# Kernel optimization log

Hardware: AMD Instinct MI355X
Metric: run time of the kernel (lower is better)

## Reference

```python
import jax, jax.numpy as jnp
import numpy as np

FEATURE_SIZE = 128
STRIDE = 16
BASE_SIZE = 16
RATIOS = [0.5, 1, 2]
SCALES = [8, 16, 32]


def _generate_anchors(feature_size, stride):
    # Faithful to the torch module's numpy anchor generation (incl. rounding).
    size = BASE_SIZE * BASE_SIZE
    size_ratios = size / np.array(RATIOS)
    ws = np.round(np.sqrt(size_ratios))
    hs = np.round(ws * np.array(RATIOS))
    base = []
    for w, h in zip(ws, hs):
        for s in SCALES:
            base.append([0.0, 0.0, w * s, h * s])
    base = np.array(base)  # [9, 4]
    xo, yo = np.meshgrid(np.arange(feature_size), np.arange(feature_size), indexing='ij')
    # original loop order: x outer, y inner, then 9 base anchors
    centers = np.stack([xo * stride, yo * stride], axis=-1).reshape(-1, 1, 2)  # [F*F,1,2]
    wh = np.broadcast_to(base[None, :, 2:4], (feature_size * feature_size, 9, 2))
    anchors = np.concatenate([np.broadcast_to(centers, wh.shape), wh], axis=-1).reshape(-1, 4)
    return jnp.asarray(anchors, dtype=jnp.float32)  # [F*F*9, 4]


def _conv(x, w, b, pad):
    y = jax.lax.conv_general_dilated(
        x, w, window_strides=(1, 1), padding=[(pad, pad), (pad, pad)],
        dimension_numbers=('NCHW', 'OIHW', 'NCHW'))
    return y + b[None, :, None, None]


def setup_inputs() -> dict:
    key = jax.random.key(0)
    ks = jax.random.split(key, 4)
    F = FEATURE_SIZE
    x = jax.random.normal(ks[0], (1, 1024, F, F), dtype=jnp.float32)
    base_w = jax.random.normal(ks[1], (512, 1024, 3, 3), dtype=jnp.float32) * 0.01
    base_b = jnp.zeros((512,), dtype=jnp.float32)
    cls_w = jax.random.normal(ks[2], (18, 512, 1, 1), dtype=jnp.float32) * 0.01
    cls_b = jnp.zeros((18,), dtype=jnp.float32)
    reg_w = jax.random.normal(ks[3], (36, 512, 1, 1), dtype=jnp.float32) * 0.01
    reg_b = jnp.zeros((36,), dtype=jnp.float32)
    return {"x": x, "base_w": base_w, "base_b": base_b,
            "cls_w": cls_w, "cls_b": cls_b, "reg_w": reg_w, "reg_b": reg_b}


def reference(x, base_w, base_b, cls_w, cls_b, reg_w, reg_b):
    F = FEATURE_SIZE
    anchors = _generate_anchors(F, STRIDE)  # [N,4], N = F*F*9

    rpn_conv = jax.nn.relu(_conv(x, base_w, base_b, pad=1))        # [1,512,F,F]
    rpn_cls = _conv(rpn_conv, cls_w, cls_b, pad=0)                  # [1,18,F,F]
    # softmax over the 2-way fg/bg axis after reshape, as in the original
    cls_rs = rpn_cls.reshape(1, 2, 9 * F, F)
    cls_prob = jax.nn.softmax(cls_rs, axis=1).reshape(1, 18, F, F)
    rpn_reg = _conv(rpn_conv, reg_w, reg_b, pad=0)                  # [1,36,F,F]

    cls = jnp.transpose(cls_prob, (0, 2, 3, 1)).reshape(-1, 2)      # [N,2]
    reg = jnp.transpose(rpn_reg, (0, 2, 3, 1)).reshape(-1, 4)       # [N,4]

    # Vectorized decode — faithful to the original per-anchor loop math:
    # p0 = ax + aw*d0 ; p1 = ay + ah*d1 ; p2 = aw + exp(d2) ; p3 = ah + exp(d3)
    p0 = anchors[:, 0] + anchors[:, 2] * reg[:, 0]
    p1 = anchors[:, 1] + anchors[:, 3] * reg[:, 1]
    p2 = anchors[:, 2] + jnp.exp(reg[:, 2])
    p3 = anchors[:, 3] + jnp.exp(reg[:, 3])
    proposals = jnp.stack([p0, p1, p2, p3], axis=-1)                # [N,4]
    scores = cls[:, 1]                                              # [N]
    return jnp.concatenate([proposals, scores[:, None]], axis=-1)   # [N,5]
```

## Files before the change

### kernel.cpp

```cpp
#include <hip/hip_runtime.h>
#include <hip/hip_bf16.h>

typedef unsigned short u16;
typedef short s8v __attribute__((ext_vector_type(8)));
typedef float f4v __attribute__((ext_vector_type(4)));

#define F 128
#define CIN 1024
#define CMID 512
#define XP 130
#define K9 9216

#define A_ELEMS 8704
#define B_ELEMS 8192
#define AOFF(b) ((b) * A_ELEMS)
#define BOFF(b) (2 * A_ELEMS + (b) * B_ELEMS)

__device__ __forceinline__ u16 f2bf(float v) {
    union { float f; unsigned u; } x; x.f = v;
    unsigned r = x.u + 0x7fff + ((x.u >> 16) & 1);
    return (u16)(r >> 16);
}
__device__ __forceinline__ float bf2f(u16 u) {
    union { unsigned u; float f; } x; x.u = ((unsigned)u) << 16; return x.f;
}

__device__ __forceinline__ void gl16(const u16* g, u16* l) {
    __builtin_amdgcn_global_load_lds(
        (const __attribute__((address_space(1))) void*)g,
        (__attribute__((address_space(3))) void*)l,
        16, 0, 0);
}

__constant__ float WBASE[9] = {184.f, 368.f, 736.f, 128.f, 256.f, 512.f,  88.f, 176.f, 352.f};
__constant__ float HBASE[9] = { 96.f, 192.f, 384.f, 128.f, 256.f, 512.f, 176.f, 352.f, 704.f};

__global__ __launch_bounds__(256) void prep_all(
    const float* __restrict__ x, const float* __restrict__ bw,
    const float* __restrict__ cls_w, const float* __restrict__ reg_w,
    u16* __restrict__ xpad, u16* __restrict__ wt, u16* __restrict__ wc) {
    __shared__ char ldsraw[128 * 65 * 4];
    const int b = blockIdx.x;
    const int tid = threadIdx.x;

    if (b < 512) {
        float (*lds)[65] = (float(*)[65])ldsraw;
        const int h  = b >> 2;
        const int c0 = (b & 3) * 256;
        #pragma unroll 1
        for (int cc = 0; cc < 4; ++cc) {
            const int cb = c0 + cc * 64;
            {
                const int w4 = (tid & 31) * 4;
                const int cl = tid >> 5;
                #pragma unroll
                for (int p = 0; p < 8; ++p) {
                    const int c = p * 8 + cl;
                    f4v v = *(const f4v*)&x[(cb + c) * (F * F) + h * F + w4];
                    #pragma unroll
                    for (int k = 0; k < 4; ++k) lds[w4 + k][c] = v[k];
                }
            }
            __syncthreads();
            {
                const int cs = (tid & 7) * 8;
                const int wb = tid >> 3;
                #pragma unroll
                for (int p = 0; p < 4; ++p) {
                    const int w = p * 32 + wb;
                    s8v v;
                    #pragma unroll
                    for (int j = 0; j < 8; ++j) v[j] = (short)f2bf(lds[w][cs + j]);
                    *(s8v*)&xpad[((h + 1) * XP + (w + 1)) * CIN + cb + cs] = v;
                }
            }
            __syncthreads();
        }
    } else if (b < 1024) {
        u16* lds = (u16*)ldsraw;
        const int oc = b - 512;
        for (int k = 0; k < 36; ++k) {
            int idx = k * 256 + tid;
            float v = bw[oc * K9 + idx];
            int c = idx / 9, q = idx - c * 9;
            lds[q * 1033 + c] = f2bf(v);
        }
        __syncthreads();
        for (int k = 0; k < 36; ++k) {
            int idx = k * 256 + tid;
            int q = idx >> 10, c = idx & 1023;
            wt[oc * K9 + idx] = lds[q * 1033 + c];
        }
    } else if (b < 1282) {
        int t = (b - 1024) * 256 + tid;
        int cell = t >> 7, c8 = (t & 127) * 8;
        int h, w;
        if (cell < 130)      { h = 0;   w = cell; }
        else if (cell < 260) { h = 129; w = cell - 130; }
        else { int rm = cell - 260; h = 1 + (rm >> 1); w = (rm & 1) * 129; }
        s8v z = {};
        *(s8v*)&xpad[(h * XP + w) * CIN + c8] = z;
    } else {
        int t = (b - 1282) * 256 + tid;
        int oc = t >> 9, c = t & 511;
        float v = 0.f;
        if (oc < 18)      v = cls_w[oc * 512 + c];
        else if (oc < 54) v = reg_w[(oc - 18) * 512 + c];
        wc[t] = f2bf(v);
    }
}

__global__ __launch_bounds__(256, 2) void gemm_conv(
    const u16* __restrict__ xpad, const u16* __restrict__ wt,
    const float* __restrict__ bias, u16* __restrict__ rpn) {
    __shared__ u16 smem[2 * A_ELEMS + 2 * B_ELEMS];
    const int tid = threadIdx.x;
    const int bid = blockIdx.x;
    const int oc0 = ((bid & 7) >> 1) * 128;
    const int gh  = (bid >> 3) * 2 + (bid & 1);

    const int lane = tid & 63;
    const int wv = tid >> 6;
    const int lm = lane & 15;
    const int lq = lane >> 4;
    const int wm = (wv >> 1) * 64;
    const int wn = (wv & 1) * 64;

    const int sw = (lane & 7) ^ ((lane >> 3) & 7);
    const u16* pA = xpad + (lane >> 3) * CIN + sw * 8;
    const u16* pB = wt + (size_t)(oc0 + wv * 32 + (lane >> 3)) * K9 + sw * 8;

    f4v acc[4][4] = {};

    auto issueA = [&](int ms) {
        const int dy = ms >> 4, cc = ms & 15;
        const u16* src = pA + ((gh + dy) * XP) * CIN + cc * 64;
        u16* dst = &smem[AOFF(ms & 1)];
        #pragma unroll
        for (int jj = 0; jj < 4; ++jj) {
            const int ci = wv * 4 + jj;
            gl16(src + ci * 8 * CIN, dst + ci * 512);
        }
        if (wv == 0) gl16(src + 16 * 8 * CIN, dst + 16 * 512);
    };
    auto issueB = [&](int ms, int dx, int buf) {
        const int dy = ms >> 4, cc = ms & 15;
        const int dydx = dy * 3 + dx;
        const u16* src = pB + dydx * CIN + cc * 64;
        u16* dst = &smem[BOFF(buf) + wv * 32 * 64];
        #pragma unroll
        for (int jj = 0; jj < 4; ++jj)
            gl16(src + jj * 8 * K9, dst + jj * 8 * 64);
    };

    issueA(0);
    issueB(0, 0, 0);
    __syncthreads();

    int t = 0;
    for (int ms = 0; ms < 48; ++ms) {
        const u16* Ab = &smem[AOFF(ms & 1)];
        #pragma unroll
        for (int dx = 0; dx < 3; ++dx, ++t) {
            if (t + 1 < 144) {
                const int msn = (dx == 2) ? ms + 1 : ms;
                const int dxn = (dx == 2) ? 0 : dx + 1;
                issueB(msn, dxn, (t + 1) & 1);
            }
            if (dx == 0 && ms + 1 < 48) issueA(ms + 1);
            const u16* Bb = &smem[BOFF(t & 1)];
            #pragma unroll
            for (int kk = 0; kk < 2; ++kk) {
                const int kseg = kk * 4 + lq;
                s8v af[4], bfr[4];
                #pragma unroll
                for (int i = 0; i < 4; ++i) {
                    const int ra = wm + i * 16 + lm + dx;
                    const int rb = wn + i * 16 + lm;
                    af[i]  = *(const s8v*)&Ab[ra * 64 + ((kseg ^ (ra & 7)) << 3)];
                    bfr[i] = *(const s8v*)&Bb[rb * 64 + ((kseg ^ (rb & 7)) << 3)];
                }
                #pragma unroll
                for (int mi = 0; mi < 4; ++mi)
                    #pragma unroll
                    for (int ni = 0; ni < 4; ++ni)
                        acc[mi][ni] = __builtin_amdgcn_mfma_f32_16x16x32_bf16(
                            af[mi], bfr[ni], acc[mi][ni], 0, 0, 0);
            }
            __syncthreads();
        }
    }

    #pragma unroll
    for (int ni = 0; ni < 4; ++ni) {
        const int oc = oc0 + wn + ni * 16 + lm;
        const float bv = bias[oc];
        #pragma unroll
        for (int mi = 0; mi < 4; ++mi) {
            #pragma unroll
            for (int rr = 0; rr < 4; ++rr) {
                const int m = wm + mi * 16 + lq * 4 + rr;
                float v = acc[mi][ni][rr] + bv;
                v = v > 0.f ? v : 0.f;
                rpn[(gh * 128 + m) * CMID + oc] = f2bf(v);
            }
        }
    }
}

__global__ __launch_bounds__(256) void stage23(
    const u16* __restrict__ rpn, const u16* __restrict__ wc,
    const float* __restrict__ cls_b, const float* __restrict__ reg_b,
    float* __restrict__ out) {
    __shared__ float part[4][16][65];
    const int tid = threadIdx.x, lane = tid & 63, wv = tid >> 6;
    const int lm = lane & 15, lq = lane >> 4;
    const int m0 = blockIdx.x * 16;

    f4v acc[4] = {};
    const u16* arow = rpn + (m0 + lm) * CMID + wv * 128 + lq * 8;
    const u16* brow = wc + lm * CMID + wv * 128 + lq * 8;
    #pragma unroll
    for (int k = 0; k < 4; ++k) {
        s8v af = *(const s8v*)(arow + k * 32);
        #pragma unroll
        for (int ni = 0; ni < 4; ++ni) {
            s8v bf = *(const s8v*)(brow + ni * 16 * CMID + k * 32);
            acc[ni] = __builtin_amdgcn_mfma_f32_16x16x32_bf16(af, bf, acc[ni], 0, 0, 0);
        }
    }
    #pragma unroll
    for (int ni = 0; ni < 4; ++ni)
        #pragma unroll
        for (int rr = 0; rr < 4; ++rr)
            part[wv][lq * 4 + rr][ni * 16 + lm] = acc[ni][rr];
    __syncthreads();

    float vsum[4];
    const int col = tid & 63, rb = tid >> 6;
    const float bv = col < 18 ? cls_b[col] : (col < 54 ? reg_b[col - 18] : 0.f);
    #pragma unroll
    for (int rr = 0; rr < 4; ++rr) {
        const int row = rb * 4 + rr;
        vsum[rr] = part[0][row][col] + part[1][row][col]
                 + part[2][row][col] + part[3][row][col] + bv;
    }
    __syncthreads();
    #pragma unroll
    for (int rr = 0; rr < 4; ++rr)
        part[0][rb * 4 + rr][col] = vsum[rr];
    __syncthreads();

    if (tid < 144) {
        const int pl = tid / 9, a = tid - pl * 9;
        const float* v = part[0][pl];
        const int ch = 2 * a + 1;
        const int pair = (ch < 9) ? ch + 9 : ch - 9;
        const float score = 1.f / (1.f + expf(v[pair] - v[ch]));
        const float r0 = v[18 + 4 * a], r1 = v[19 + 4 * a];
        const float r2 = v[20 + 4 * a], r3 = v[21 + 4 * a];
        const float wb = WBASE[a], hb = HBASE[a];
        const int p = m0 + pl;
        const int h = p >> 7, w = p & 127;
        float* o = out + (p * 9 + a) * 5;
        o[0] = h * 16.f + wb * r0;
        o[1] = w * 16.f + hb * r1;
        o[2] = wb + expf(r2);
        o[3] = hb + expf(r3);
        o[4] = score;
    }
}

extern "C" void kernel_launch(void* const* d_in, const int* in_sizes, int n_in,
                              void* d_out, int out_size, void* d_ws, size_t ws_size,
                              hipStream_t stream) {
    const float* x      = (const float*)d_in[0];
    const float* base_w = (const float*)d_in[1];
    const float* base_b = (const float*)d_in[2];
    const float* cls_w  = (const float*)d_in[3];
    const float* cls_b  = (const float*)d_in[4];
    const float* reg_w  = (const float*)d_in[5];
    const float* reg_b  = (const float*)d_in[6];
    float* out = (float*)d_out;

    char* ws = (char*)d_ws;
    u16* xpad = (u16*)ws;
    u16* wt   = (u16*)(ws + 34611200);
    u16* wc   = (u16*)(ws + 34611200 + 9437184);
    u16* rpn  = (u16*)(ws + 34611200 + 9437184 + 65536);

    prep_all<<<1410, 256, 0, stream>>>(x, base_w, cls_w, reg_w, xpad, wt, wc);
    gemm_conv<<<512, 256, 0, stream>>>(xpad, wt, base_b, rpn);
    stage23<<<1024, 256, 0, stream>>>(rpn, wc, cls_b, reg_b, out);
}
```

Baseline: 259.6 us.

## Load weight fragments directly into registers from a pre-swizzled layout, dropping B LDS staging

The prep kernel now writes the 3x3 conv weights in a fragment-ordered layout, so each lane can load its MFMA B operands straight from global memory into registers. The GEMM drops the double-buffered B tiles in LDS, keeps a three-slot register ring of B fragments prefetched one dx step ahead, and syncs once per channel chunk instead of once per dx. This removes LDS traffic and two of every three barriers, and halves LDS use. In exchange it adds about 96 VGPRs for the B fragments, which could hurt the two-waves-per-SIMD occupancy target or cause spills, and puts the B loads on L2/global latency.

```diff
diff --git a/kernel.cpp b/kernel.cpp
--- a/kernel.cpp
+++ b/kernel.cpp
@@ -12,9 +12,7 @@
 #define K9 9216
 
 #define A_ELEMS 8704
-#define B_ELEMS 8192
 #define AOFF(b) ((b) * A_ELEMS)
-#define BOFF(b) (2 * A_ELEMS + (b) * B_ELEMS)
 
 __device__ __forceinline__ u16 f2bf(float v) {
     union { float f; unsigned u; } x; x.f = v;
@@ -38,7 +36,7 @@
 __global__ __launch_bounds__(256) void prep_all(
     const float* __restrict__ x, const float* __restrict__ bw,
     const float* __restrict__ cls_w, const float* __restrict__ reg_w,
-    u16* __restrict__ xpad, u16* __restrict__ wt, u16* __restrict__ wc) {
+    u16* __restrict__ xpad, u16* __restrict__ wt2, u16* __restrict__ wc) {
     __shared__ char ldsraw[128 * 65 * 4];
     const int b = blockIdx.x;
     const int tid = threadIdx.x;
@@ -79,6 +77,7 @@
     } else if (b < 1024) {
         u16* lds = (u16*)ldsraw;
         const int oc = b - 512;
+        const int nb = oc >> 7, nf = (oc >> 4) & 7, lmo = oc & 15;
         for (int k = 0; k < 36; ++k) {
             int idx = k * 256 + tid;
             float v = bw[oc * K9 + idx];
@@ -86,10 +85,16 @@
             lds[q * 1033 + c] = f2bf(v);
         }
         __syncthreads();
-        for (int k = 0; k < 36; ++k) {
-            int idx = k * 256 + tid;
-            int q = idx >> 10, c = idx & 1023;
-            wt[oc * K9 + idx] = lds[q * 1033 + c];
+        u16* dst = wt2 + (size_t)nb * 1179648 + nf * 512 + lmo * 8;
+        for (int t2 = tid; t2 < 1152; t2 += 256) {
+            int dydx = t2 >> 7;
+            int r = t2 & 127;
+            int cc = r >> 3, kk = (r >> 2) & 1, lq = r & 3;
+            int cbase = cc * 64 + kk * 32 + lq * 8;
+            s8v v;
+            #pragma unroll
+            for (int j = 0; j < 8; ++j) v[j] = (short)lds[dydx * 1033 + cbase + j];
+            *(s8v*)&dst[dydx * 131072 + cc * 8192 + kk * 4096 + lq * 128] = v;
         }
     } else if (b < 1282) {
         int t = (b - 1024) * 256 + tid;
@@ -111,12 +116,13 @@
 }
 
 __global__ __launch_bounds__(256, 2) void gemm_conv(
-    const u16* __restrict__ xpad, const u16* __restrict__ wt,
+    const u16* __restrict__ xpad, const u16* __restrict__ wt2,
     const float* __restrict__ bias, u16* __restrict__ rpn) {
-    __shared__ u16 smem[2 * A_ELEMS + 2 * B_ELEMS];
+    __shared__ u16 smem[2 * A_ELEMS];
     const int tid = threadIdx.x;
     const int bid = blockIdx.x;
-    const int oc0 = ((bid & 7) >> 1) * 128;
+    const int nb  = (bid & 7) >> 1;
+    const int oc0 = nb * 128;
     const int gh  = (bid >> 3) * 2 + (bid & 1);
 
     const int lane = tid & 63;
@@ -128,9 +134,10 @@
 
     const int sw = (lane & 7) ^ ((lane >> 3) & 7);
     const u16* pA = xpad + (lane >> 3) * CIN + sw * 8;
-    const u16* pB = wt + (size_t)(oc0 + wv * 32 + (lane >> 3)) * K9 + sw * 8;
+    const u16* pB2 = wt2 + (size_t)nb * 1179648 + (wv & 1) * 2048 + lane * 8;
 
     f4v acc[4][4] = {};
+    s8v breg[3][8];
 
     auto issueA = [&](int ms) {
         const int dy = ms >> 4, cc = ms & 15;
@@ -143,52 +150,50 @@
         }
         if (wv == 0) gl16(src + 16 * 8 * CIN, dst + 16 * 512);
     };
-    auto issueB = [&](int ms, int dx, int buf) {
+    auto loadB = [&](int dydx, int cc, int buf) {
+        const u16* src = pB2 + dydx * 131072 + cc * 8192;
+        #pragma unroll
+        for (int kk = 0; kk < 2; ++kk)
+            #pragma unroll
+            for (int ni = 0; ni < 4; ++ni)
+                breg[buf][kk * 4 + ni] = *(const s8v*)(src + kk * 4096 + ni * 512);
+    };
+
+    issueA(0);
+    loadB(0, 0, 0);
+    loadB(1, 0, 1);
+    __syncthreads();
+
+    for (int ms = 0; ms < 48; ++ms) {
         const int dy = ms >> 4, cc = ms & 15;
-        const int dydx = dy * 3 + dx;
-        const u16* src = pB + dydx * CIN + cc * 64;
-        u16* dst = &smem[BOFF(buf) + wv * 32 * 64];
-        #pragma unroll
-        for (int jj = 0; jj < 4; ++jj)
-            gl16(src + jj * 8 * K9, dst + jj * 8 * 64);
-    };
-
-    issueA(0);
-    issueB(0, 0, 0);
-    __syncthreads();
-
-    int t = 0;
-    for (int ms = 0; ms < 48; ++ms) {
+        if (ms + 1 < 48) issueA(ms + 1);
         const u16* Ab = &smem[AOFF(ms & 1)];
         #pragma unroll
-        for (int dx = 0; dx < 3; ++dx, ++t) {
-            if (t + 1 < 144) {
-                const int msn = (dx == 2) ? ms + 1 : ms;
-                const int dxn = (dx == 2) ? 0 : dx + 1;
-                issueB(msn, dxn, (t + 1) & 1);
-            }
-            if (dx == 0 && ms + 1 < 48) issueA(ms + 1);
-            const u16* Bb = &smem[BOFF(t & 1)];
+        for (int dx = 0; dx < 3; ++dx) {
+            if (dx == 0) {
+                loadB(dy * 3 + 2, cc, 2);
+            } else if (ms + 1 < 48) {
+                const int dyn = (ms + 1) >> 4, ccn = (ms + 1) & 15;
+                loadB(dyn * 3 + (dx - 1), ccn, (dx + 2) % 3);
+            }
             #pragma unroll
             for (int kk = 0; kk < 2; ++kk) {
                 const int kseg = kk * 4 + lq;
-                s8v af[4], bfr[4];
+                s8v af[4];
                 #pragma unroll
                 for (int i = 0; i < 4; ++i) {
                     const int ra = wm + i * 16 + lm + dx;
-                    const int rb = wn + i * 16 + lm;
-                    af[i]  = *(const s8v*)&Ab[ra * 64 + ((kseg ^ (ra & 7)) << 3)];
-                    bfr[i] = *(const s8v*)&Bb[rb * 64 + ((kseg ^ (rb & 7)) << 3)];
+                    af[i] = *(const s8v*)&Ab[ra * 64 + ((kseg ^ (ra & 7)) << 3)];
                 }
                 #pragma unroll
                 for (int mi = 0; mi < 4; ++mi)
                     #pragma unroll
                     for (int ni = 0; ni < 4; ++ni)
                         acc[mi][ni] = __builtin_amdgcn_mfma_f32_16x16x32_bf16(
-                            af[mi], bfr[ni], acc[mi][ni], 0, 0, 0);
-            }
-            __syncthreads();
-        }
+                            af[mi], breg[dx][kk * 4 + ni], acc[mi][ni], 0, 0, 0);
+            }
+        }
+        __syncthreads();
     }
 
     #pragma unroll
@@ -285,11 +290,11 @@
 
     char* ws = (char*)d_ws;
     u16* xpad = (u16*)ws;
-    u16* wt   = (u16*)(ws + 34611200);
+    u16* wt2  = (u16*)(ws + 34611200);
     u16* wc   = (u16*)(ws + 34611200 + 9437184);
     u16* rpn  = (u16*)(ws + 34611200 + 9437184 + 65536);
 
-    prep_all<<<1410, 256, 0, stream>>>(x, base_w, cls_w, reg_w, xpad, wt, wc);
-    gemm_conv<<<512, 256, 0, stream>>>(xpad, wt, base_b, rpn);
+    prep_all<<<1410, 256, 0, stream>>>(x, base_w, cls_w, reg_w, xpad, wt2, wc);
+    gemm_conv<<<512, 256, 0, stream>>>(xpad, wt2, base_b, rpn);
     stage23<<<1024, 256, 0, stream>>>(rpn, wc, cls_b, reg_b, out);
 }
```

Result: slower. 275.4 us (+6.1%).
